# Performance work log

Hardware: AMD Instinct MI355X
Metric: run time of the kernel (lower is better)

Reference implementation:

```python
import jax, jax.numpy as jnp
import numpy as np
import math

NUM_BUCKETS = 32
MAX_DISTANCE = 128

def _next_pow2(n):
    return 1 << (int(n) - 1).bit_length()

def _rel_pos_bucket(rel_pos):
    # causal T5 bucket: n = max(q - k, 0)
    n = jnp.maximum(-rel_pos, 0)
    max_exact = NUM_BUCKETS // 2
    is_small = n < max_exact
    n_safe = jnp.maximum(n, 1).astype(jnp.float32)
    val_if_large = max_exact + (
        jnp.log(n_safe / max_exact) / math.log(MAX_DISTANCE / max_exact) * (NUM_BUCKETS - max_exact)
    ).astype(jnp.int32)
    val_if_large = jnp.minimum(val_if_large, NUM_BUCKETS - 1)
    return jnp.where(is_small, n, val_if_large)

def setup_inputs() -> dict:
    key = jax.random.key(0)
    ks = jax.random.split(key, 20)
    B, L, D = 8, 2048, 128
    H, DQK, DV = 16, 64, 256
    s = 0.05
    return {
        'x': jax.random.normal(ks[0], (B, L, D), jnp.float32),
        'expansion': jax.random.normal(ks[1], (H, D), jnp.float32) * s,
        'reduction': jax.random.normal(ks[2], (H, D), jnp.float32) * s,
        'alphas': jax.random.normal(ks[3], (H,), jnp.float32),
        'dampen_factors': jax.random.normal(ks[4], (H,), jnp.float32),
        'rel_bias': jax.random.normal(ks[5], (NUM_BUCKETS, 1), jnp.float32) * s,
        'W_qk': jax.random.normal(ks[6], (D, DQK), jnp.float32) * s,
        'b_qk': jnp.zeros((DQK,), jnp.float32),
        'gamma': jax.random.normal(ks[7], (2, DQK), jnp.float32) * 0.02 + 1.0,
        'beta': jnp.zeros((2, DQK), jnp.float32),
        'W_v': jax.random.normal(ks[8], (D, DV), jnp.float32) * s,
        'b_v': jnp.zeros((DV,), jnp.float32),
        'W_reset': jax.random.normal(ks[9], (D, DV), jnp.float32) * s,
        'b_reset': jnp.zeros((DV,), jnp.float32),
        'W_update': jax.random.normal(ks[10], (D, D), jnp.float32) * s,
        'b_update': jnp.zeros((D,), jnp.float32),
        'Wh': jax.random.normal(ks[11], (D, D), jnp.float32) * s,
        'Uh': jax.random.normal(ks[12], (DV, D), jnp.float32) * s,
        'bh': jnp.zeros((D,), jnp.float32),
    }

def reference(x, expansion, reduction, alphas, dampen_factors, rel_bias,
              W_qk, b_qk, gamma, beta, W_v, b_v, W_reset, b_reset,
              W_update, b_update, Wh, Uh, bh):
    B, L, D = x.shape
    DQK = W_qk.shape[1]
    # ---- MultiHeadedEMA (causal, FFT conv) ----
    xe = jnp.einsum('bnd,hd->bnhd', x, expansion)  # [B,L,H,D]
    a = jax.nn.sigmoid(alphas)
    damp = jax.nn.sigmoid(dampen_factors)
    t = jnp.arange(L, dtype=x.dtype)
    kern = a[:, None] * ((1.0 - a) * damp)[:, None] ** t[None, :]  # [H,L]
    fft_len = _next_pow2(2 * L - 1)
    Xf = jnp.fft.rfft(xe, n=fft_len, axis=1)           # [B,F,H,D]
    Kf = jnp.fft.rfft(kern, n=fft_len, axis=-1)        # [H,F]
    y = jnp.fft.irfft(Xf * Kf.T[None, :, :, None], n=fft_len, axis=1)[:, :L]
    ema = jnp.einsum('bnhd,hd->bnd', y, reduction)     # [B,L,D]
    # ---- SingleHeadedAttention(ema, v_input=x) ----
    qk = jax.nn.silu(ema @ W_qk + b_qk)                # [B,L,DQK]
    q = qk * gamma[0] + beta[0]
    k = qk * gamma[1] + beta[1]
    v = jax.nn.silu(x @ W_v + b_v)                     # [B,L,DV]
    scale = D ** -0.5
    sim = jnp.einsum('bid,bjd->bij', q, k) * scale
    pos = jnp.arange(L)
    rel = pos[None, :] - pos[:, None]                  # [L,L] j - i
    bias = rel_bias[_rel_pos_bucket(rel), 0] * (DQK ** 0.5)
    sim = sim + bias
    sim = jnp.where(rel > 0, jnp.finfo(sim.dtype).min, sim)  # strict causal mask
    attn = jax.nn.softmax(sim, axis=-1)
    attn_out = jnp.einsum('bij,bjd->bid', attn, v)     # [B,L,DV]
    # ---- gating ----
    reset_gate = jax.nn.silu(ema @ W_reset + b_reset)
    update_gate = jax.nn.sigmoid(ema @ W_update + b_update)
    gated = attn_out * reset_gate
    Hh = jax.nn.silu(ema @ Wh + gated @ Uh + bh)
    return update_gate * Hh + (1.0 - update_gate) * x
```

## Files before the change

### kernel.cpp

```cpp
#include <hip/hip_runtime.h>
#include <hip/hip_bf16.h>
#include <math.h>

#define BB 8
#define LL 2048
#define DD 128
#define DQKN 64
#define DVN 256
#define MTOT (BB*LL)
#define SCALE 0.08838834764831845f
#define LOG2E 1.4426950408889634f
#define QSCALE (SCALE*LOG2E)

#define CHUNK 32
#define NCH (LL/CHUNK)
#define CT 4
#define NCHK 144

typedef __attribute__((ext_vector_type(4))) float f32x4;
typedef __attribute__((ext_vector_type(8))) short s16x8;

__device__ __forceinline__ float sigmoidf_(float x){ return 1.f/(1.f+__expf(-x)); }
__device__ __forceinline__ float siluf_(float x){ return x/(1.f+__expf(-x)); }
__device__ __forceinline__ __hip_bfloat16 f2bf(float f){ return __float2bfloat16(f); }
__device__ __forceinline__ ushort f2bfu(float f){ __hip_bfloat16 h = __float2bfloat16(f); return *(const ushort*)&h; }
__device__ __forceinline__ float bf2f(ushort u){ union{unsigned i; float f;} v; v.i = ((unsigned)u)<<16; return v.f; }

__device__ __forceinline__ void gl_lds16(const __hip_bfloat16* g, void* l) {
    __builtin_amdgcn_global_load_lds(
        (const __attribute__((address_space(1))) void*)g,
        (__attribute__((address_space(3))) void*)l, 16, 0, 0);
}

__global__ void pack_all(const float* __restrict__ Wqk, const float* __restrict__ Wv,
                         const float* __restrict__ Wrst, const float* __restrict__ Wu,
                         const float* __restrict__ Wh, const float* __restrict__ Uh,
                         const float* __restrict__ rel_bias,
                         __hip_bfloat16* __restrict__ WqkP, __hip_bfloat16* __restrict__ WvP,
                         __hip_bfloat16* __restrict__ WrstP, __hip_bfloat16* __restrict__ WuP,
                         __hip_bfloat16* __restrict__ WhP, __hip_bfloat16* __restrict__ UhP,
                         float* __restrict__ btab) {
    int blk = blockIdx.x;
    int l = threadIdx.x;
    if (blk == 272) {
        for (int n = l; n < LL; n += 64) {
            int bucket;
            if (n < 16) bucket = n;
            else {
                float v = logf((float)n * (1.0f/16.0f)) * (1.0f/logf(8.0f)) * 16.0f;
                bucket = 16 + (int)v;
                if (bucket > 31) bucket = 31;
            }
            btab[n] = rel_bias[bucket] * 8.0f * LOG2E;
        }
        return;
    }
    const float* W; __hip_bfloat16* Wp; int K, N;
    if (blk < 16)       { W=Wqk;  Wp=WqkP;  K=128; N=64; }
    else if (blk < 80)  { W=Wv;   Wp=WvP;   K=128; N=256; blk-=16; }
    else if (blk < 144) { W=Wrst; Wp=WrstP; K=128; N=256; blk-=80; }
    else if (blk < 176) { W=Wu;   Wp=WuP;   K=128; N=128; blk-=144; }
    else if (blk < 208) { W=Wh;   Wp=WhP;   K=128; N=128; blk-=176; }
    else                { W=Uh;   Wp=UhP;   K=256; N=128; blk-=208; }
    int k32 = blk % (K/32), n16 = blk / (K/32);
    int col = n16*16 + (l & 15);
    int krow = k32*32 + (l >> 4)*8;
    ushort tmp[8];
    #pragma unroll
    for (int j = 0; j < 8; ++j) tmp[j] = f2bfu(W[(size_t)(krow + j)*N + col]);
    *reinterpret_cast<uint4*>(Wp + ((size_t)blk*64 + l)*8) = *reinterpret_cast<uint4*>(tmp);
}

__global__ __launch_bounds__(256) void ema_scanA(const float* __restrict__ x,
                                                 const float* __restrict__ alphas,
                                                 const float* __restrict__ damps,
                                                 float* __restrict__ sl) {
    int tid = blockIdx.x * 256 + threadIdx.x;
    int d = tid & 127;
    int c = (tid >> 7) & (NCH - 1);
    int b = tid >> 13;
    float u[16], r[16];
    #pragma unroll
    for (int h = 0; h < 16; ++h) {
        float a = sigmoidf_(alphas[h]);
        r[h] = (1.f - a) * sigmoidf_(damps[h]);
        u[h] = 0.f;
    }
    const float* xp = x + ((size_t)b * LL + c * CHUNK) * DD + d;
    #pragma unroll 4
    for (int i = 0; i < CHUNK; ++i) {
        float xv = xp[(size_t)i * DD];
        #pragma unroll
        for (int h = 0; h < 16; ++h) u[h] = fmaf(r[h], u[h], xv);
    }
    float* slp = sl + ((size_t)b * NCH + c) * 16 * DD + d;
    #pragma unroll
    for (int h = 0; h < 16; ++h) slp[(size_t)h * DD] = u[h];
}

__global__ __launch_bounds__(256) void ema_scanB(const float* __restrict__ alphas,
                                                 const float* __restrict__ damps,
                                                 const float* __restrict__ sl,
                                                 float* __restrict__ carry) {
    int tid = blockIdx.x * 256 + threadIdx.x;
    int d = tid & 127;
    int h = (tid >> 7) & 15;
    int b = tid >> 11;
    float a = sigmoidf_(alphas[h]);
    float r = (1.f - a) * sigmoidf_(damps[h]);
    float rC = r;
    #pragma unroll
    for (int q = 0; q < 5; ++q) rC *= rC;
    const float* slp = sl + ((size_t)b * NCH * 16 + h) * DD + d;
    float* cp = carry + ((size_t)b * NCH * 16 + h) * DD + d;
    float u = 0.f;
    for (int c = 0; c < NCH; ++c) {
        cp[(size_t)c * 16 * DD] = u;
        u = slp[(size_t)c * 16 * DD] + rC * u;
    }
}

__global__ __launch_bounds__(256) void ema_scanC(const float* __restrict__ x,
                                                 const float* __restrict__ expansion,
                                                 const float* __restrict__ reduction,
                                                 const float* __restrict__ alphas,
                                                 const float* __restrict__ damps,
                                                 const float* __restrict__ carry,
                                                 __hip_bfloat16* __restrict__ emab,
                                                 __hip_bfloat16* __restrict__ xb) {
    int tid = blockIdx.x * 256 + threadIdx.x;
    int d = tid & 127;
    int c = (tid >> 7) & (NCH - 1);
    int b = tid >> 13;
    float u[16], r[16], we[16];
    #pragma unroll
    for (int h = 0; h < 16; ++h) {
        float a = sigmoidf_(alphas[h]);
        r[h] = (1.f - a) * sigmoidf_(damps[h]);
        we[h] = reduction[h * DD + d] * a * expansion[h * DD + d];
        u[h] = carry[((size_t)b * NCH + c) * 16 * DD + (size_t)h * DD + d];
    }
    const float* xp = x + ((size_t)b * LL + c * CHUNK) * DD + d;
    __hip_bfloat16* ep = emab + ((size_t)b * LL + c * CHUNK) * DD + d;
    __hip_bfloat16* xbp = xb + ((size_t)b * LL + c * CHUNK) * DD + d;
    #pragma unroll 4
    for (int i = 0; i < CHUNK; ++i) {
        float xv = xp[(size_t)i * DD];
        float acc = 0.f;
        #pragma unroll
        for (int h = 0; h < 16; ++h) {
            u[h] = fmaf(r[h], u[h], xv);
            acc = fmaf(we[h], u[h], acc);
        }
        ep[(size_t)i * DD] = f2bf(acc);
        xbp[(size_t)i * DD] = f2bf(xv);
    }
}

__global__ __launch_bounds__(256) void gemm_qk(const __hip_bfloat16* __restrict__ A,
        const __hip_bfloat16* __restrict__ Wp, const float* __restrict__ bias,
        const float* __restrict__ gamma, const float* __restrict__ beta,
        __hip_bfloat16* __restrict__ qb, __hip_bfloat16* __restrict__ kb) {
    __shared__ char AsB[64*256];
    const int row0 = blockIdx.x * 64;
    const int t = threadIdx.x, w = t>>6, lane = t&63, l16 = lane&15, l4 = lane>>4;
    #pragma unroll
    for (int p = 0; p < 4; ++p) {
        int idx = p*256 + t;
        int row = idx / 16, u = idx % 16;
        uint4 d = *reinterpret_cast<const uint4*>(A + (size_t)(row0+row)*DD + u*8);
        *reinterpret_cast<uint4*>(AsB + row*256 + ((u*16) ^ ((row&7)<<4))) = d;
    }
    __syncthreads();
    f32x4 acc[4];
    #pragma unroll
    for (int n = 0; n < 4; ++n) acc[n] = (f32x4){0.f,0.f,0.f,0.f};
    const int arow = w*16 + l16;
    #pragma unroll
    for (int k32 = 0; k32 < 4; ++k32) {
        s16x8 af = *reinterpret_cast<const s16x8*>(AsB + arow*256 + ((k32*64 + l4*16) ^ ((arow&7)<<4)));
        #pragma unroll
        for (int n = 0; n < 4; ++n) {
            s16x8 bfr = *reinterpret_cast<const s16x8*>(Wp + ((size_t)(n*4 + k32)*64 + lane)*8);
            acc[n] = __builtin_amdgcn_mfma_f32_16x16x32_bf16(af, bfr, acc[n], 0, 0, 0);
        }
    }
    #pragma unroll
    for (int n = 0; n < 4; ++n) {
        int col = n*16 + l16;
        float bb = bias[col];
        float g0 = gamma[col], g1 = gamma[DQKN + col];
        float be0 = beta[col], be1 = beta[DQKN + col];
        #pragma unroll
        for (int r = 0; r < 4; ++r) {
            int row = w*16 + l4*4 + r;
            float s = siluf_(acc[n][r] + bb);
            qb[(size_t)(row0+row)*DQKN + col] = f2bf((s*g0 + be0) * QSCALE);
            kb[(size_t)(row0+row)*DQKN + col] = f2bf(s*g1 + be1);
        }
    }
}

__global__ __launch_bounds__(256) void gemm_vrst(const __hip_bfloat16* __restrict__ xb,
        const __hip_bfloat16* __restrict__ emab,
        const __hip_bfloat16* __restrict__ WvP, const __hip_bfloat16* __restrict__ WrstP,
        const float* __restrict__ b_v, const float* __restrict__ b_rst,
        __hip_bfloat16* __restrict__ vT, __hip_bfloat16* __restrict__ rstb) {
    __shared__ char AsB[64*256];
    const int mode = blockIdx.y;
    const __hip_bfloat16* A = mode ? emab : xb;
    const __hip_bfloat16* Wp = mode ? WrstP : WvP;
    const float* bias = mode ? b_rst : b_v;
    const int row0 = blockIdx.x * 64;
    const int t = threadIdx.x, w = t>>6, lane = t&63, l16 = lane&15, l4 = lane>>4;
    #pragma unroll
    for (int p = 0; p < 4; ++p) {
        int idx = p*256 + t;
        int row = idx / 16, u = idx % 16;
        uint4 d = *reinterpret_cast<const uint4*>(A + (size_t)(row0+row)*DD + u*8);
        *reinterpret_cast<uint4*>(AsB + row*256 + ((u*16) ^ ((row&7)<<4))) = d;
    }
    __syncthreads();
    f32x4 acc[16];
    #pragma unroll
    for (int n = 0; n < 16; ++n) acc[n] = (f32x4){0.f,0.f,0.f,0.f};
    const int arow = w*16 + l16;
    #pragma unroll
    for (int k32 = 0; k32 < 4; ++k32) {
        s16x8 af = *reinterpret_cast<const s16x8*>(AsB + arow*256 + ((k32*64 + l4*16) ^ ((arow&7)<<4)));
        #pragma unroll
        for (int n = 0; n < 16; ++n) {
            s16x8 bfr = *reinterpret_cast<const s16x8*>(Wp + ((size_t)(n*4 + k32)*64 + lane)*8);
            acc[n] = __builtin_amdgcn_mfma_f32_16x16x32_bf16(af, bfr, acc[n], 0, 0, 0);
        }
    }
    if (mode == 0) {
        int bb_i = row0 >> 11;
        int lpos0 = (row0 & 2047) + w*16 + l4*4;
        #pragma unroll
        for (int n = 0; n < 16; ++n) {
            int col = n*16 + l16;
            float bb = bias[col];
            ushort pk[4];
            #pragma unroll
            for (int r = 0; r < 4; ++r) pk[r] = f2bfu(siluf_(acc[n][r] + bb));
            *reinterpret_cast<ushort4*>(vT + ((size_t)bb_i*DVN + col)*LL + lpos0) = *reinterpret_cast<ushort4*>(pk);
        }
    } else {
        #pragma unroll
        for (int n = 0; n < 16; ++n) {
            int col = n*16 + l16;
            float bb = bias[col];
            #pragma unroll
            for (int r = 0; r < 4; ++r) {
                int row = w*16 + l4*4 + r;
                rstb[(size_t)(row0+row)*DVN + col] = f2bf(siluf_(acc[n][r] + bb));
            }
        }
    }
}

__global__ __launch_bounds__(256) void attn_kernel(
    const __hip_bfloat16* __restrict__ qg, const __hip_bfloat16* __restrict__ kg,
    const __hip_bfloat16* __restrict__ vTg, const float* __restrict__ btab,
    __hip_bfloat16* __restrict__ aob, __hip_bfloat16* __restrict__ part_o,
    float* __restrict__ part_ml) {
    __shared__ __hip_bfloat16 Ks[64 * 64];
    __shared__ __hip_bfloat16 Vs[256 * 64];
    __shared__ __hip_bfloat16 Ps[4][16][72];
    __shared__ float btl[320];
    const int cid = NCHK - 1 - (int)blockIdx.x;
    const int b = blockIdx.y;
    int g = 0;
    while (cid >= 2*(g+1)*(g+2)) ++g;
    const int rel = cid - 2*g*(g+1);
    const int ti = 4*g + rel/(g+1);
    const int cch = rel % (g+1);
    const int i0 = ti * 64;
    const int jlo = cch * (CT*64);
    int jhi = jlo + CT*64; { int je = (ti+1)*64; if (jhi > je) jhi = je; }
    const int nt = (jhi - jlo) >> 6;
    const int t = threadIdx.x;
    const int w = t >> 6, lane = t & 63;
    const int l16 = lane & 15, l4 = lane >> 4;
    char* KsB = (char*)Ks;
    char* VsB = (char*)Vs;

    int dmin = i0 - jhi + 1; if (dmin < 0) dmin = 0;
    const int cnt = (i0 + 63 - jlo) - dmin + 1;
    for (int idx = t; idx < cnt; idx += 256) btl[idx] = btab[dmin + idx];

    const int irow = i0 + w * 16 + l16;
    s16x8 qf[2];
    qf[0] = *reinterpret_cast<const s16x8*>(qg + ((size_t)b * LL + irow) * DQKN + l4 * 8);
    qf[1] = *reinterpret_cast<const s16x8*>(qg + ((size_t)b * LL + irow) * DQKN + 32 + l4 * 8);

    f32x4 o[16];
    #pragma unroll
    for (int n16 = 0; n16 < 16; ++n16) o[n16] = (f32x4){0.f, 0.f, 0.f, 0.f};
    float m[4] = {-1e30f, -1e30f, -1e30f, -1e30f};
    float l[4] = {0.f, 0.f, 0.f, 0.f};

    for (int tt = 0; tt < nt; ++tt) {
        const int j0 = jlo + tt * 64;
        __syncthreads();
        #pragma unroll
        for (int i = 0; i < 2; ++i) {
            int base = w * 128 + i * 64;
            int idx = base + lane;
            int row = idx >> 3;
            int c16 = (idx & 7) ^ (row & 7);
            gl_lds16(kg + ((size_t)b * LL + j0 + row) * DQKN + c16 * 8, KsB + base * 16);
        }
        #pragma unroll
        for (int i = 0; i < 8; ++i) {
            int base = w * 512 + i * 64;
            int idx = base + lane;
            int n = idx >> 3;
            int c16 = (idx & 7) ^ (n & 7);
            gl_lds16(vTg + ((size_t)b * DVN + n) * LL + j0 + c16 * 8, VsB + base * 16);
        }
        __syncthreads();
        f32x4 s[4];
        #pragma unroll
        for (int t16 = 0; t16 < 4; ++t16) s[t16] = (f32x4){0.f, 0.f, 0.f, 0.f};
        #pragma unroll
        for (int c = 0; c < 2; ++c) {
            #pragma unroll
            for (int t16 = 0; t16 < 4; ++t16) {
                int j = t16 * 16 + l16;
                s16x8 kf = *reinterpret_cast<const s16x8*>(KsB + j * 128 + ((c * 64 + l4 * 16) ^ ((j & 7) << 4)));
                s[t16] = __builtin_amdgcn_mfma_f32_16x16x32_bf16(qf[c], kf, s[t16], 0, 0, 0);
            }
        }
        float sv[4][4];
        float rmax[4] = {-1e30f, -1e30f, -1e30f, -1e30f};
        #pragma unroll
        for (int t16 = 0; t16 < 4; ++t16) {
            #pragma unroll
            for (int r = 0; r < 4; ++r) {
                int row = l4 * 4 + r;
                int dlt = (i0 + w * 16 + row) - (j0 + t16 * 16 + l16);
                int bi = dlt - dmin; if (bi < 0) bi = 0;
                float bv = btl[bi];
                float val = (dlt >= 0) ? (s[t16][r] + bv) : -1e30f;
                sv[t16][r] = val;
                rmax[r] = fmaxf(rmax[r], val);
            }
        }
        #pragma unroll
        for (int off = 1; off < 16; off <<= 1) {
            #pragma unroll
            for (int r = 0; r < 4; ++r) rmax[r] = fmaxf(rmax[r], __shfl_xor(rmax[r], off));
        }
        bool need = (rmax[0] > m[0]) || (rmax[1] > m[1]) || (rmax[2] > m[2]) || (rmax[3] > m[3]);
        if (__any(need)) {
            float alpha[4];
            #pragma unroll
            for (int r = 0; r < 4; ++r) {
                float mn = fmaxf(m[r], rmax[r]);
                alpha[r] = exp2f(m[r] - mn);
                m[r] = mn;
                l[r] *= alpha[r];
            }
            #pragma unroll
            for (int n16 = 0; n16 < 16; ++n16) {
                #pragma unroll
                for (int r = 0; r < 4; ++r) o[n16][r] *= alpha[r];
            }
        }
        float psum[4] = {0.f, 0.f, 0.f, 0.f};
        #pragma unroll
        for (int t16 = 0; t16 < 4; ++t16) {
            #pragma unroll
            for (int r = 0; r < 4; ++r) {
                float p = exp2f(sv[t16][r] - m[r]);
                psum[r] += p;
                Ps[w][l4 * 4 + r][t16 * 16 + l16] = f2bf(p);
            }
        }
        #pragma unroll
        for (int off = 1; off < 16; off <<= 1) {
            #pragma unroll
            for (int r = 0; r < 4; ++r) psum[r] += __shfl_xor(psum[r], off);
        }
        #pragma unroll
        for (int r = 0; r < 4; ++r) l[r] += psum[r];
        #pragma unroll
        for (int c = 0; c < 2; ++c) {
            s16x8 pf = *reinterpret_cast<const s16x8*>(&Ps[w][l16][c * 32 + l4 * 8]);
            #pragma unroll
            for (int n16 = 0; n16 < 16; ++n16) {
                int n = n16 * 16 + l16;
                s16x8 vf = *reinterpret_cast<const s16x8*>(VsB + n * 128 + ((c * 64 + l4 * 16) ^ ((n & 7) << 4)));
                o[n16] = __builtin_amdgcn_mfma_f32_16x16x32_bf16(pf, vf, o[n16], 0, 0, 0);
            }
        }
    }
    if (ti < 4) {
        float invl[4];
        #pragma unroll
        for (int r = 0; r < 4; ++r) invl[r] = 1.f / l[r];
        #pragma unroll
        for (int n16 = 0; n16 < 16; ++n16) {
            #pragma unroll
            for (int r = 0; r < 4; ++r) {
                aob[((size_t)b * LL + i0 + w * 16 + l4 * 4 + r) * DVN + n16 * 16 + l16] = f2bf(o[n16][r] * invl[r]);
            }
        }
    } else {
        const size_t slot = (size_t)b * NCHK + cid;
        __hip_bfloat16* po = part_o + slot * (64 * 256);
        #pragma unroll
        for (int n16 = 0; n16 < 16; ++n16) {
            #pragma unroll
            for (int r = 0; r < 4; ++r)
                po[(size_t)(w * 16 + l4 * 4 + r) * 256 + n16 * 16 + l16] = f2bf(o[n16][r]);
        }
        if (l16 == 0) {
            #pragma unroll
            for (int r = 0; r < 4; ++r) {
                int row = w * 16 + l4 * 4 + r;
                part_ml[slot * 128 + row * 2]     = m[r];
                part_ml[slot * 128 + row * 2 + 1] = l[r];
            }
        }
    }
}

__global__ __launch_bounds__(256) void attn_combine(const __hip_bfloat16* __restrict__ part_o,
                                                    const float* __restrict__ part_ml,
                                                    __hip_bfloat16* __restrict__ aob) {
    const int ti = 4 + (int)blockIdx.x;
    const int ch = blockIdx.y;
    const int b = blockIdx.z;
    const int g = ti >> 2;
    const int nc = g + 1;
    const int cid0 = 2*g*(g+1) + (ti - 4*g)*(g+1);
    const size_t slot0 = (size_t)b * NCHK + cid0;
    __shared__ float sW[8][64];
    __shared__ float sinvL[64];
    const int t = threadIdx.x;
    if (t < 64) {
        float M = -1e30f;
        for (int c = 0; c < nc; ++c)
            M = fmaxf(M, part_ml[(slot0 + c) * 128 + t * 2]);
        float L = 0.f;
        for (int c = 0; c < nc; ++c) {
            float wv = exp2f(part_ml[(slot0 + c) * 128 + t * 2] - M);
            sW[c][t] = wv;
            L += wv * part_ml[(slot0 + c) * 128 + t * 2 + 1];
        }
        sinvL[t] = 1.f / L;
    }
    __syncthreads();
    const int i0 = ti * 64;
    #pragma unroll
    for (int it = 0; it < 4; ++it) {
        int idx = it * 256 + t;
        int row = idx >> 4, c8 = idx & 15;
        int colu = ch * 16 + c8;
        float acc[8] = {0.f,0.f,0.f,0.f,0.f,0.f,0.f,0.f};
        for (int c = 0; c < nc; ++c) {
            float wv = sW[c][row];
            uint4 d = *reinterpret_cast<const uint4*>(part_o + (slot0 + c) * (size_t)(64*256) + row * 256 + colu * 8);
            const ushort* pp = (const ushort*)&d;
            #pragma unroll
            for (int j = 0; j < 8; ++j) acc[j] = fmaf(wv, bf2f(pp[j]), acc[j]);
        }
        float il = sinvL[row];
        ushort pk[8];
        #pragma unroll
        for (int j = 0; j < 8; ++j) pk[j] = f2bfu(acc[j] * il);
        *reinterpret_cast<uint4*>(aob + ((size_t)b * LL + i0 + row) * DVN + colu * 8) = *reinterpret_cast<uint4*>(pk);
    }
}

__global__ __launch_bounds__(256) void final_mfma(
        const __hip_bfloat16* __restrict__ emab, const __hip_bfloat16* __restrict__ aob,
        const __hip_bfloat16* __restrict__ rstb, const float* __restrict__ x,
        const __hip_bfloat16* __restrict__ WhP, const __hip_bfloat16* __restrict__ UhP,
        const __hip_bfloat16* __restrict__ WuP, const float* __restrict__ bh,
        const float* __restrict__ bu, float* __restrict__ out) {
    __shared__ char As1[64*256];
    __shared__ char As2[64*512];
    const int row0 = blockIdx.x * 64;
    const int ch = blockIdx.y;
    const int t = threadIdx.x, w = t>>6, lane = t&63, l16 = lane&15, l4 = lane>>4;
    #pragma unroll
    for (int p = 0; p < 4; ++p) {
        int idx = p*256 + t;
        int row = idx / 16, u = idx % 16;
        uint4 d = *reinterpret_cast<const uint4*>(emab + (size_t)(row0+row)*DD + u*8);
        *reinterpret_cast<uint4*>(As1 + row*256 + ((u*16) ^ ((row&7)<<4))) = d;
    }
    #pragma unroll
    for (int p = 0; p < 8; ++p) {
        int idx = p*256 + t;
        int row = idx / 32, u = idx % 32;
        uint4 da = *reinterpret_cast<const uint4*>(aob + (size_t)(row0+row)*DVN + u*8);
        uint4 dr = *reinterpret_cast<const uint4*>(rstb + (size_t)(row0+row)*DVN + u*8);
        const ushort* pa = (const ushort*)&da;
        const ushort* pr = (const ushort*)&dr;
        ushort gg[8];
        #pragma unroll
        for (int j = 0; j < 8; ++j) gg[j] = f2bfu(bf2f(pa[j]) * bf2f(pr[j]));
        *reinterpret_cast<uint4*>(As2 + row*512 + ((u*16) ^ ((row&7)<<4))) = *reinterpret_cast<uint4*>(gg);
    }
    __syncthreads();
    f32x4 acc1[4], acc2[4];
    #pragma unroll
    for (int n = 0; n < 4; ++n) { acc1[n] = (f32x4){0.f,0.f,0.f,0.f}; acc2[n] = (f32x4){0.f,0.f,0.f,0.f}; }
    const int arow = w*16 + l16;
    #pragma unroll
    for (int k32 = 0; k32 < 4; ++k32) {
        s16x8 af = *reinterpret_cast<const s16x8*>(As1 + arow*256 + ((k32*64 + l4*16) ^ ((arow&7)<<4)));
        #pragma unroll
        for (int n = 0; n < 4; ++n) {
            s16x8 bw = *reinterpret_cast<const s16x8*>(WhP + ((size_t)((ch*4+n)*4 + k32)*64 + lane)*8);
            acc1[n] = __builtin_amdgcn_mfma_f32_16x16x32_bf16(af, bw, acc1[n], 0, 0, 0);
            s16x8 bu2 = *reinterpret_cast<const s16x8*>(WuP + ((size_t)((ch*4+n)*4 + k32)*64 + lane)*8);
            acc2[n] = __builtin_amdgcn_mfma_f32_16x16x32_bf16(af, bu2, acc2[n], 0, 0, 0);
        }
    }
    #pragma unroll
    for (int k32 = 0; k32 < 8; ++k32) {
        s16x8 gf = *reinterpret_cast<const s16x8*>(As2 + arow*512 + ((k32*64 + l4*16) ^ ((arow&7)<<4)));
        #pragma unroll
        for (int n = 0; n < 4; ++n) {
            s16x8 bw = *reinterpret_cast<const s16x8*>(UhP + ((size_t)((ch*4+n)*8 + k32)*64 + lane)*8);
            acc1[n] = __builtin_amdgcn_mfma_f32_16x16x32_bf16(gf, bw, acc1[n], 0, 0, 0);
        }
    }
    #pragma unroll
    for (int n = 0; n < 4; ++n) {
        int col = ch*64 + n*16 + l16;
        float bbh = bh[col], bbu = bu[col];
        #pragma unroll
        for (int r = 0; r < 4; ++r) {
            int row = w*16 + l4*4 + r;
            size_t gidx = (size_t)(row0+row)*DD + col;
            float hh = siluf_(acc1[n][r] + bbh);
            float u = sigmoidf_(acc2[n][r] + bbu);
            float xv = x[gidx];
            out[gidx] = u*hh + (1.f-u)*xv;
        }
    }
}

extern "C" void kernel_launch(void* const* d_in, const int* in_sizes, int n_in,
                              void* d_out, int out_size, void* d_ws, size_t ws_size,
                              hipStream_t stream) {
    const float* x        = (const float*)d_in[0];
    const float* expansion= (const float*)d_in[1];
    const float* reduction= (const float*)d_in[2];
    const float* alphas   = (const float*)d_in[3];
    const float* damps    = (const float*)d_in[4];
    const float* rel_bias = (const float*)d_in[5];
    const float* W_qk     = (const float*)d_in[6];
    const float* b_qk     = (const float*)d_in[7];
    const float* gamma    = (const float*)d_in[8];
    const float* beta     = (const float*)d_in[9];
    const float* W_v      = (const float*)d_in[10];
    const float* b_v      = (const float*)d_in[11];
    const float* W_reset  = (const float*)d_in[12];
    const float* b_reset  = (const float*)d_in[13];
    const float* W_update = (const float*)d_in[14];
    const float* b_update = (const float*)d_in[15];
    const float* Wh       = (const float*)d_in[16];
    const float* Uh       = (const float*)d_in[17];
    const float* bh       = (const float*)d_in[18];
    float* out = (float*)d_out;

    char* base = (char*)d_ws;
    __hip_bfloat16* emab = (__hip_bfloat16*)base;  base += (size_t)MTOT * DD * 2;
    __hip_bfloat16* xb   = (__hip_bfloat16*)base;  base += (size_t)MTOT * DD * 2;
    __hip_bfloat16* qb   = (__hip_bfloat16*)base;  base += (size_t)MTOT * DQKN * 2;
    __hip_bfloat16* kb   = (__hip_bfloat16*)base;  base += (size_t)MTOT * DQKN * 2;
    __hip_bfloat16* vT   = (__hip_bfloat16*)base;  base += (size_t)MTOT * DVN * 2;
    __hip_bfloat16* rstb = (__hip_bfloat16*)base;  base += (size_t)MTOT * DVN * 2;
    __hip_bfloat16* aob  = (__hip_bfloat16*)base;  base += (size_t)MTOT * DVN * 2;
    float* btab  = (float*)base;                   base += (size_t)LL * 4;
    float* sl    = (float*)base;                   base += (size_t)BB * NCH * 16 * DD * 4;
    float* carry = (float*)base;                   base += (size_t)BB * NCH * 16 * DD * 4;
    __hip_bfloat16* WqkP = (__hip_bfloat16*)base;  base += (size_t)DD * DQKN * 2;
    __hip_bfloat16* WvP  = (__hip_bfloat16*)base;  base += (size_t)DD * DVN * 2;
    __hip_bfloat16* WrstP= (__hip_bfloat16*)base;  base += (size_t)DD * DVN * 2;
    __hip_bfloat16* WuP  = (__hip_bfloat16*)base;  base += (size_t)DD * DD * 2;
    __hip_bfloat16* WhP  = (__hip_bfloat16*)base;  base += (size_t)DD * DD * 2;
    __hip_bfloat16* UhP  = (__hip_bfloat16*)base;  base += (size_t)DVN * DD * 2;
    __hip_bfloat16* part_o = (__hip_bfloat16*)base; base += (size_t)BB * NCHK * 64 * 256 * 2;
    float* part_ml = (float*)base;                 base += (size_t)BB * NCHK * 128 * 4;

    pack_all<<<273, 64, 0, stream>>>(W_qk, W_v, W_reset, W_update, Wh, Uh, rel_bias,
                                     WqkP, WvP, WrstP, WuP, WhP, UhP, btab);

    ema_scanA<<<BB * NCH * DD / 256, 256, 0, stream>>>(x, alphas, damps, sl);
    ema_scanB<<<BB * 16 * DD / 256, 256, 0, stream>>>(alphas, damps, sl, carry);
    ema_scanC<<<BB * NCH * DD / 256, 256, 0, stream>>>(x, expansion, reduction, alphas, damps, carry, emab, xb);

    gemm_qk<<<MTOT/64, 256, 0, stream>>>(emab, WqkP, b_qk, gamma, beta, qb, kb);
    gemm_vrst<<<dim3(MTOT/64, 2), 256, 0, stream>>>(xb, emab, WvP, WrstP, b_v, b_reset, vT, rstb);

    attn_kernel<<<dim3(NCHK, BB), 256, 0, stream>>>(qb, kb, vT, btab, aob, part_o, part_ml);
    attn_combine<<<dim3(28, 2, BB), 256, 0, stream>>>(part_o, part_ml, aob);

    final_mfma<<<dim3(MTOT/64, 2), 256, 0, stream>>>(emab, aob, rstb, x, WhP, UhP, WuP, bh, b_update, out);
}
```

Measured before the change: 120.9 us.

## Double-buffer K/V tiles in attention and fold causal mask into bias table

The attention kernel now keeps two LDS buffers for K and V and issues the async global-to-LDS loads for the next 64-key tile before computing on the current one, leaving a single barrier per iteration. This overlaps memory latency with MFMA work. Separately, the causal mask is baked into the bias table as -1e30 for negative offsets, so the inner loop does one indexed table load instead of clamping and comparing per element. LDS use roughly doubles (about 80KB), which may lower occupancy, and the safety of the prefetch relies on the global loads landing in a buffer that is not still being read.

```diff
diff --git a/kernel.cpp b/kernel.cpp
--- a/kernel.cpp
+++ b/kernel.cpp
@@ -265,8 +265,8 @@
     const __hip_bfloat16* __restrict__ vTg, const float* __restrict__ btab,
     __hip_bfloat16* __restrict__ aob, __hip_bfloat16* __restrict__ part_o,
     float* __restrict__ part_ml) {
-    __shared__ __hip_bfloat16 Ks[64 * 64];
-    __shared__ __hip_bfloat16 Vs[256 * 64];
+    __shared__ __hip_bfloat16 Ks[2][64 * 64];
+    __shared__ __hip_bfloat16 Vs[2][256 * 64];
     __shared__ __hip_bfloat16 Ps[4][16][72];
     __shared__ float btl[320];
     const int cid = NCHK - 1 - (int)blockIdx.x;
@@ -286,9 +286,12 @@
     char* KsB = (char*)Ks;
     char* VsB = (char*)Vs;
 
-    int dmin = i0 - jhi + 1; if (dmin < 0) dmin = 0;
-    const int cnt = (i0 + 63 - jlo) - dmin + 1;
-    for (int idx = t; idx < cnt; idx += 256) btl[idx] = btab[dmin + idx];
+    const int dminE = i0 - jhi + 1;
+    const int cnt = (i0 + 63 - jlo) - dminE + 1;
+    for (int idx = t; idx < cnt; idx += 256) {
+        int dlt = dminE + idx;
+        btl[idx] = (dlt >= 0) ? btab[dlt] : -1e30f;
+    }
 
     const int irow = i0 + w * 16 + l16;
     s16x8 qf[2];
@@ -301,26 +304,27 @@
     float m[4] = {-1e30f, -1e30f, -1e30f, -1e30f};
     float l[4] = {0.f, 0.f, 0.f, 0.f};
 
+    #define STAGE(BUF, J0) { \
+        _Pragma("unroll") for (int i = 0; i < 2; ++i) { \
+            int base = w * 128 + i * 64; \
+            int idx = base + lane; \
+            int row = idx >> 3; \
+            int c16 = (idx & 7) ^ (row & 7); \
+            gl_lds16(kg + ((size_t)b * LL + (J0) + row) * DQKN + c16 * 8, KsB + (BUF)*8192 + base * 16); } \
+        _Pragma("unroll") for (int i = 0; i < 8; ++i) { \
+            int base = w * 512 + i * 64; \
+            int idx = base + lane; \
+            int n = idx >> 3; \
+            int c16 = (idx & 7) ^ (n & 7); \
+            gl_lds16(vTg + ((size_t)b * DVN + n) * LL + (J0) + c16 * 8, VsB + (BUF)*32768 + base * 16); } }
+
+    STAGE(0, jlo);
+    __syncthreads();
+
     for (int tt = 0; tt < nt; ++tt) {
         const int j0 = jlo + tt * 64;
-        __syncthreads();
-        #pragma unroll
-        for (int i = 0; i < 2; ++i) {
-            int base = w * 128 + i * 64;
-            int idx = base + lane;
-            int row = idx >> 3;
-            int c16 = (idx & 7) ^ (row & 7);
-            gl_lds16(kg + ((size_t)b * LL + j0 + row) * DQKN + c16 * 8, KsB + base * 16);
-        }
-        #pragma unroll
-        for (int i = 0; i < 8; ++i) {
-            int base = w * 512 + i * 64;
-            int idx = base + lane;
-            int n = idx >> 3;
-            int c16 = (idx & 7) ^ (n & 7);
-            gl_lds16(vTg + ((size_t)b * DVN + n) * LL + j0 + c16 * 8, VsB + base * 16);
-        }
-        __syncthreads();
+        const int cur = tt & 1;
+        if (tt + 1 < nt) STAGE(cur ^ 1, j0 + 64);
         f32x4 s[4];
         #pragma unroll
         for (int t16 = 0; t16 < 4; ++t16) s[t16] = (f32x4){0.f, 0.f, 0.f, 0.f};
@@ -329,21 +333,18 @@
             #pragma unroll
             for (int t16 = 0; t16 < 4; ++t16) {
                 int j = t16 * 16 + l16;
-                s16x8 kf = *reinterpret_cast<const s16x8*>(KsB + j * 128 + ((c * 64 + l4 * 16) ^ ((j & 7) << 4)));
+                s16x8 kf = *reinterpret_cast<const s16x8*>(KsB + cur*8192 + j * 128 + ((c * 64 + l4 * 16) ^ ((j & 7) << 4)));
                 s[t16] = __builtin_amdgcn_mfma_f32_16x16x32_bf16(qf[c], kf, s[t16], 0, 0, 0);
             }
         }
+        const int Cb = (i0 + w * 16 + l4 * 4) - (j0 + l16) - dminE;
         float sv[4][4];
         float rmax[4] = {-1e30f, -1e30f, -1e30f, -1e30f};
         #pragma unroll
         for (int t16 = 0; t16 < 4; ++t16) {
             #pragma unroll
             for (int r = 0; r < 4; ++r) {
-                int row = l4 * 4 + r;
-                int dlt = (i0 + w * 16 + row) - (j0 + t16 * 16 + l16);
-                int bi = dlt - dmin; if (bi < 0) bi = 0;
-                float bv = btl[bi];
-                float val = (dlt >= 0) ? (s[t16][r] + bv) : -1e30f;
+                float val = s[t16][r] + btl[Cb + r - t16 * 16];
                 sv[t16][r] = val;
                 rmax[r] = fmaxf(rmax[r], val);
             }
@@ -392,11 +393,13 @@
             #pragma unroll
             for (int n16 = 0; n16 < 16; ++n16) {
                 int n = n16 * 16 + l16;
-                s16x8 vf = *reinterpret_cast<const s16x8*>(VsB + n * 128 + ((c * 64 + l4 * 16) ^ ((n & 7) << 4)));
+                s16x8 vf = *reinterpret_cast<const s16x8*>(VsB + cur*32768 + n * 128 + ((c * 64 + l4 * 16) ^ ((n & 7) << 4)));
                 o[n16] = __builtin_amdgcn_mfma_f32_16x16x32_bf16(pf, vf, o[n16], 0, 0, 0);
             }
         }
-    }
+        __syncthreads();
+    }
+    #undef STAGE
     if (ti < 4) {
         float invl[4];
         #pragma unroll
```

Result: slower. 136.9 us (+13.2%).
